# Performance work log

Measured on AMD Instinct MI355X. Metric: run time of the kernel, lower is better.

## Reference

```python
import jax, jax.numpy as jnp
import numpy as np

D_MODEL = 2048
NUM_HEADS = 16
THETA = 10000.0


def setup_inputs() -> dict:
    key = jax.random.key(0)
    ks = jax.random.split(key, 5)
    bs, S, d = 4, 2048, D_MODEL
    std = (2.0 / (d + d)) ** 0.5
    x = jax.random.normal(ks[0], (bs, S, d), dtype=jnp.float32)
    wq = jax.random.normal(ks[1], (d, d), dtype=jnp.float32) * std
    wk = jax.random.normal(ks[2], (d, d), dtype=jnp.float32) * std
    wv = jax.random.normal(ks[3], (d, d), dtype=jnp.float32) * std
    wo = jax.random.normal(ks[4], (d, d), dtype=jnp.float32) * std
    return {"x": x, "wq": wq, "wk": wk, "wv": wv, "wo": wo}


def _rope(t, cos, sin):
    # t: (bs, H, S, d_k); cos/sin: (S, d_k) interleaved-duplicated
    # rotate_half: (-x1, x0, -x3, x2, ...)
    x_even = t[..., 0::2]
    x_odd = t[..., 1::2]
    rot = jnp.stack((-x_odd, x_even), axis=-1).reshape(t.shape)
    return t * cos + rot * sin


def reference(x, wq, wk, wv, wo):
    bs, S, d = x.shape
    H = NUM_HEADS
    dk = d // H
    # QKV projections (Linear has no bias; weight stored (out, in), applied as x @ W.T)
    q = (x @ wq.T).reshape(bs, S, H, dk).transpose(0, 2, 1, 3)  # (bs,H,S,dk)
    k = (x @ wk.T).reshape(bs, S, H, dk).transpose(0, 2, 1, 3)
    v = (x @ wv.T).reshape(bs, S, H, dk).transpose(0, 2, 1, 3)

    # RoPE tables (interleaved convention)
    half = dk // 2
    inv_freq = THETA ** (-2.0 * jnp.arange(half, dtype=jnp.float32) / dk)  # (half,)
    pos = jnp.arange(S, dtype=jnp.float32)
    ang = pos[:, None] * inv_freq[None, :]  # (S, half)
    cos = jnp.repeat(jnp.cos(ang), 2, axis=-1)  # (S, dk), (c0,c0,c1,c1,...)
    sin = jnp.repeat(jnp.sin(ang), 2, axis=-1)
    q = _rope(q, cos, sin)
    k = _rope(k, cos, sin)

    scale = 1.0 / jnp.sqrt(jnp.asarray(dk, dtype=x.dtype))
    attn = jnp.einsum("bhqd,bhkd->bhqk", q, k) * scale  # (bs,H,S,S)
    causal = jnp.tril(jnp.ones((S, S), dtype=bool))
    attn = jnp.where(causal, attn, -jnp.inf)
    probs = jax.nn.softmax(attn, axis=-1)
    out = jnp.einsum("bhqk,bhkd->bhqd", probs, v)  # (bs,H,S,dk)
    out = out.transpose(0, 2, 1, 3).reshape(bs, S, d)
    return out @ wo.T
```

## Files before the change

### kernel.cpp

```cpp
#include <hip/hip_runtime.h>
#include <hip/hip_bf16.h>
#include <cstdint>
#include <cstddef>

typedef unsigned short u16;
typedef unsigned int u32;
typedef __attribute__((ext_vector_type(8))) short short8;
typedef __attribute__((ext_vector_type(4))) short bfx4;
typedef __attribute__((ext_vector_type(4))) float f32x4;

#define D_MODEL 2048
#define SEQ     2048
#define BATCH   4
#define NHEADS  16
#define DKH     128
#define NTOK    (BATCH*SEQ)

typedef const __attribute__((address_space(1))) void* gptr_t;
typedef __attribute__((address_space(3))) void* lptr_t;

__device__ inline float bf2f(u16 u) {
  union { float f; u32 i; } x; x.i = ((u32)u) << 16; return x.f;
}
__device__ inline u16 f2bf(float f) {
  union { float f; u32 i; } x; x.f = f;
  return (u16)((x.i + 0x7FFFu + ((x.i >> 16) & 1u)) >> 16);
}
__device__ inline u32 packbf2(float a, float b) {
  union { float f; u32 i; } xa, xb; xa.f = a; xb.f = b;
  return (xa.i >> 16) | (xb.i & 0xFFFF0000u);
}

__global__ void cvt_kernel(const float* __restrict__ in, u16* __restrict__ out, int n8) {
  int i = blockIdx.x * 256 + threadIdx.x;
  if (i >= n8) return;
  const float* p = in + (size_t)i * 8;
  short8 v;
#pragma unroll
  for (int j = 0; j < 8; ++j) v[j] = (short)f2bf(p[j]);
  *(short8*)(out + (size_t)i * 8) = v;
}

__global__ void cvtw_kernel(const float* __restrict__ wq, const float* __restrict__ wk,
                            const float* __restrict__ wv, const float* __restrict__ wo,
                            u16* __restrict__ wall) {
  int by = blockIdx.y;
  const float* src = by == 0 ? wq : by == 1 ? wk : by == 2 ? wv : wo;
  int i = blockIdx.x * 256 + threadIdx.x;
  const float* p = src + (size_t)i * 8;
  short8 v;
#pragma unroll
  for (int j = 0; j < 8; ++j) v[j] = (short)f2bf(p[j]);
  *(short8*)(wall + (size_t)by * D_MODEL * D_MODEL + (size_t)i * 8) = v;
}

__global__ void trig_kernel(float* __restrict__ cosT, float* __restrict__ sinT) {
  int i = blockIdx.x * 256 + threadIdx.x;
  int s = i >> 6, j = i & 63;
  float inv = powf(10000.0f, -2.0f * (float)j / 128.0f);
  float ang = (float)s * inv;
  cosT[i] = cosf(ang);
  sinT[i] = sinf(ang);
}

template<int F32OUT>
__global__ __launch_bounds__(512, 2)
void gemm_bt256(const u16* __restrict__ A, const u16* __restrict__ B,
                void* __restrict__ Cv, int M, int N, int K) {
  __shared__ u16 lds[2][2][256 * 64];
  const int T = threadIdx.x;
  const int lane = T & 63, w = T >> 6;
  const int lo = lane & 15, hi = lane >> 4;
  const int wr = w >> 2, wc = w & 3;
  const int id = blockIdx.x;
  const int bm = (id >> 3) * 256, bn = (id & 7) * 256;
  const int nt = K >> 6;

  const int qrow_base = (w & 3) * 8 + (w >> 2) * 128;
  const int lrow = lane >> 3;
  const int lchunk = lane & 7;

  auto STAGEQ = [&](int buf, int z, int kt) {
    int r0 = z * 32 + qrow_base;
    int rn = r0 + lrow;
    int ck = lchunk ^ (rn & 7);
    __builtin_amdgcn_global_load_lds(
        (gptr_t)(A + (size_t)(bm + rn) * K + kt * 64 + ck * 8),
        (lptr_t)(&lds[buf][0][0] + r0 * 64), 16, 0, 0);
    __builtin_amdgcn_global_load_lds(
        (gptr_t)(B + (size_t)(bn + rn) * K + kt * 64 + ck * 8),
        (lptr_t)(&lds[buf][1][0] + r0 * 64), 16, 0, 0);
  };

  f32x4 acc[8][4] = {};
  short8 bfrag[4][2];

#define GPHASE(qq, tt, cc) do {                                                \
    short8 af[2][2];                                                           \
    _Pragma("unroll")                                                          \
    for (int m2 = 0; m2 < 2; ++m2) {                                           \
      int row = wr * 128 + (2 * (qq) + m2) * 16 + lo;                          \
      _Pragma("unroll")                                                        \
      for (int c = 0; c < 2; ++c)                                              \
        af[m2][c] = *(const short8*)((const char*)&lds[cc][0][0] +             \
            (row << 7) + ((c * 64 + hi * 16) ^ ((row & 7) << 4)));             \
    }                                                                          \
    if ((qq) == 0) {                                                           \
      _Pragma("unroll")                                                        \
      for (int ni = 0; ni < 4; ++ni) {                                         \
        int row = wc * 64 + ni * 16 + lo;                                      \
        _Pragma("unroll")                                                      \
        for (int c = 0; c < 2; ++c)                                            \
          bfrag[ni][c] = *(const short8*)((const char*)&lds[cc][1][0] +        \
              (row << 7) + ((c * 64 + hi * 16) ^ ((row & 7) << 4)));           \
      }                                                                        \
    }                                                                          \
    { int zz = ((qq) + 3) & 3;                                                 \
      int stt = (qq) == 0 ? (tt) + 1 : (tt) + 2;                               \
      int sbuf = (qq) == 0 ? ((tt) + 1) & 1 : (tt) & 1;                        \
      if (stt < nt) STAGEQ(sbuf, zz, stt); }                                   \
    __builtin_amdgcn_s_barrier();                                              \
    asm volatile("s_waitcnt lgkmcnt(0)" ::: "memory");                         \
    __builtin_amdgcn_sched_barrier(0);                                         \
    __builtin_amdgcn_s_setprio(1);                                             \
    _Pragma("unroll")                                                          \
    for (int m2 = 0; m2 < 2; ++m2)                                             \
      _Pragma("unroll")                                                        \
      for (int ni = 0; ni < 4; ++ni)                                           \
        _Pragma("unroll")                                                      \
        for (int c = 0; c < 2; ++c)                                            \
          acc[2 * (qq) + m2][ni] = __builtin_amdgcn_mfma_f32_16x16x32_bf16(    \
              af[m2][c], bfrag[ni][c], acc[2 * (qq) + m2][ni], 0, 0, 0);       \
    __builtin_amdgcn_s_setprio(0);                                             \
    __builtin_amdgcn_sched_barrier(0);                                         \
    __builtin_amdgcn_s_barrier();                                              \
  } while (0)

#pragma unroll
  for (int z = 0; z < 4; ++z) STAGEQ(0, z, 0);
#pragma unroll
  for (int z = 0; z < 3; ++z) STAGEQ(1, z, 1);
  asm volatile("s_waitcnt vmcnt(6)" ::: "memory");
  __builtin_amdgcn_s_barrier();

  for (int t = 0; t < nt; ++t) {
    const int cur = t & 1;
    GPHASE(0, t, cur);
    GPHASE(1, t, cur);
    GPHASE(2, t, cur);
    GPHASE(3, t, cur);
    if (t == nt - 2) asm volatile("s_waitcnt vmcnt(0)" ::: "memory");
    else             asm volatile("s_waitcnt vmcnt(6)" ::: "memory");
    __builtin_amdgcn_s_barrier();
  }
#undef GPHASE

#pragma unroll
  for (int mi = 0; mi < 8; ++mi)
#pragma unroll
    for (int ni = 0; ni < 4; ++ni) {
      int row = bm + wr * 128 + mi * 16 + hi * 4;
      int col = bn + wc * 64 + ni * 16 + lo;
#pragma unroll
      for (int r = 0; r < 4; ++r) {
        if (F32OUT)
          ((float*)Cv)[(size_t)(row + r) * N + col] = acc[mi][ni][r];
        else
          ((u16*)Cv)[(size_t)(row + r) * N + col] = f2bf(acc[mi][ni][r]);
      }
    }
}

__global__ void rope_kernel(u16* __restrict__ t, const float* __restrict__ cosT,
                            const float* __restrict__ sinT, float premul) {
  int i = blockIdx.x * 256 + threadIdx.x;
  int row = i >> 8;
  int g = i & 255;
  int s = row & (SEQ - 1);
  int col = g << 3;
  int j0 = (col & 127) >> 1;
  short8 v = *(short8*)(t + (size_t)row * D_MODEL + col);
#pragma unroll
  for (int p = 0; p < 4; ++p) {
    float c  = cosT[s * 64 + j0 + p];
    float sn = sinT[s * 64 + j0 + p];
    float e = bf2f((u16)v[2 * p]), o = bf2f((u16)v[2 * p + 1]);
    v[2 * p]     = (short)f2bf((e * c - o * sn) * premul);
    v[2 * p + 1] = (short)f2bf((o * c + e * sn) * premul);
  }
  *(short8*)(t + (size_t)row * D_MODEL + col) = v;
}

__global__ void vt_kernel(const u16* __restrict__ V, u16* __restrict__ VT) {
  __shared__ u16 tbuf[64][66];
  int bh = blockIdx.z;
  int b = bh >> 4, h = bh & 15;
  int s0 = blockIdx.x << 6, d0 = blockIdx.y << 6;
  for (int i = threadIdx.x; i < 512; i += 256) {
    int sr = i >> 3, c8 = (i & 7) << 3;
    short8 v = *(const short8*)(V + (size_t)(b * SEQ + s0 + sr) * D_MODEL + h * DKH + d0 + c8);
#pragma unroll
    for (int j = 0; j < 8; ++j) tbuf[sr][c8 + j] = (u16)v[j];
  }
  __syncthreads();
  for (int i = threadIdx.x; i < 512; i += 256) {
    int dr = i >> 3, s8 = (i & 7) << 3;
    short8 v;
#pragma unroll
    for (int j = 0; j < 8; ++j) v[j] = (short)tbuf[s8 + j][dr];
    *(short8*)(VT + ((size_t)bh * DKH + d0 + dr) * SEQ + s0 + s8) = v;
  }
}

__device__ __forceinline__ void attn_band(
    int band, int b, int h, int bh,
    const u16* __restrict__ Q, const u16* __restrict__ K,
    const u16* __restrict__ VT, u16* __restrict__ O,
    const float* __restrict__ cosT, const float* __restrict__ sinT,
    u16 (*Ksb)[64 * 128], u16 (*Vsb)[128 * 64], u16* Pw)
{
  const int T = threadIdx.x, lane = T & 63, w = T >> 6;
  const int lo = lane & 15, hi = lane >> 4;
  const int grp = w >> 2, wl = w & 3;
  const int qt = band * 2 + grp;
  const int qrow = qt * 64 + wl * 16 + lo;
  const int ktmax = band * 2 + 1;
  const int swzC = (lo & 7) << 4;
  const float SC = 0.08838834764831845f * 1.4426950408889634f;

  const u16* Qp = Q + (size_t)(b * SEQ + qrow) * D_MODEL + h * DKH;
  const float* cp = cosT + qrow * 64;
  const float* sp = sinT + qrow * 64;
  short8 qf[4];
#pragma unroll
  for (int c = 0; c < 4; ++c) {
    short8 v = *(const short8*)(Qp + c * 32 + hi * 8);
#pragma unroll
    for (int p = 0; p < 4; ++p) {
      float cc = cp[c * 16 + hi * 4 + p] * SC;
      float sn = sp[c * 16 + hi * 4 + p] * SC;
      float e = bf2f((u16)v[2 * p]), o = bf2f((u16)v[2 * p + 1]);
      v[2 * p]     = (short)f2bf(e * cc - o * sn);
      v[2 * p + 1] = (short)f2bf(o * cc + e * sn);
    }
    qf[c] = v;
  }

  f32x4 ot[8] = {};
  float m = -1e30f, l = 0.f;

  const u16* Kbase = K + ((size_t)b * SEQ) * D_MODEL + h * DKH;
  const u16* Vbase = VT + (size_t)bh * DKH * SEQ;

  auto STAGE = [&](int buf, int kt2) {
    const int kb2 = kt2 << 6;
#pragma unroll
    for (int q = 0; q < 2; ++q) {
      int base = q * 512 + w * 64;
      int s = base + lane;
      int kv = s >> 4, ck = (s & 15) ^ (kv & 7);
      __builtin_amdgcn_global_load_lds(
          (gptr_t)(Kbase + (size_t)(kb2 + kv) * D_MODEL + ck * 8),
          (lptr_t)(Ksb[buf] + (size_t)base * 8), 16, 0, 0);
      int d = s >> 3, cv2 = (s & 7) ^ (d & 7);
      __builtin_amdgcn_global_load_lds(
          (gptr_t)(Vbase + (size_t)d * SEQ + kb2 + cv2 * 8),
          (lptr_t)(Vsb[buf] + (size_t)base * 8), 16, 0, 0);
    }
  };

  STAGE(0, 0);
  __syncthreads();
  int cur = 0;

  for (int kt = 0; kt <= ktmax; ++kt) {
    if (kt < ktmax) STAGE(cur ^ 1, kt + 1);
    if (kt <= qt) {
      const int kb = kt << 6;
      const u16* Ks = Ksb[cur];
      const u16* Vs = Vsb[cur];

      f32x4 sa[4];
      __builtin_amdgcn_s_setprio(1);
#pragma unroll
      for (int g = 0; g < 4; ++g) {
        f32x4 s4 = {0.f, 0.f, 0.f, 0.f};
        int krow = g * 16 + lo;
#pragma unroll
        for (int c = 0; c < 4; ++c) {
          int o = ((krow << 8) + c * 64 + hi * 16) ^ ((krow & 7) << 4);
          short8 kf = *(const short8*)((const char*)Ks + o);
          s4 = __builtin_amdgcn_mfma_f32_16x16x32_bf16(kf, qf[c], s4, 0, 0, 0);
        }
        sa[g] = s4;
      }
      __builtin_amdgcn_s_setprio(0);

      const bool diag = (kt == qt);
      float pm = -1e30f;
#pragma unroll
      for (int g = 0; g < 4; ++g)
#pragma unroll
        for (int r = 0; r < 4; ++r) {
          float sv = sa[g][r];
          if (diag && (kb + g * 16 + hi * 4 + r) > qrow) sv = -1e30f;
          sa[g][r] = sv;
          pm = fmaxf(pm, sv);
        }
      pm = fmaxf(pm, __shfl_xor(pm, 16));
      pm = fmaxf(pm, __shfl_xor(pm, 32));

      if (!__all(pm <= m + 8.0f)) {
        float mn = fmaxf(m, pm);
        float sc = __builtin_amdgcn_exp2f(m - mn);
        l *= sc;
#pragma unroll
        for (int g2 = 0; g2 < 8; ++g2)
#pragma unroll
          for (int r = 0; r < 4; ++r) ot[g2][r] *= sc;
        m = mn;
      }

      float rs = 0.f;
#pragma unroll
      for (int g = 0; g < 4; ++g) {
        float p0 = __builtin_amdgcn_exp2f(sa[g][0] - m);
        float p1 = __builtin_amdgcn_exp2f(sa[g][1] - m);
        float p2 = __builtin_amdgcn_exp2f(sa[g][2] - m);
        float p3 = __builtin_amdgcn_exp2f(sa[g][3] - m);
        rs += (p0 + p1) + (p2 + p3);
        int off = lo * 128 + ((g * 32 + hi * 8) ^ swzC);
        *(u32*)((char*)Pw + off)     = packbf2(p0, p1);
        *(u32*)((char*)Pw + off + 4) = packbf2(p2, p3);
      }
      rs += __shfl_xor(rs, 16);
      rs += __shfl_xor(rs, 32);
      l += rs;

      __builtin_amdgcn_s_setprio(1);
#pragma unroll
      for (int c2 = 0; c2 < 2; ++c2) {
        short8 pf = *(const short8*)((char*)Pw + lo * 128 + ((c2 * 64 + hi * 16) ^ swzC));
#pragma unroll
        for (int g2 = 0; g2 < 8; ++g2) {
          int vrow = g2 * 16 + lo;
          int vo = ((vrow << 7) + c2 * 64 + hi * 16) ^ ((vrow & 7) << 4);
          short8 vf = *(const short8*)((const char*)Vs + vo);
          ot[g2] = __builtin_amdgcn_mfma_f32_16x16x32_bf16(vf, pf, ot[g2], 0, 0, 0);
        }
      }
      __builtin_amdgcn_s_setprio(0);
    }

    __syncthreads();
    cur ^= 1;
  }

  float invl = 1.0f / l;
  u16* Op = O + (size_t)(b * SEQ + qrow) * D_MODEL + h * DKH + hi * 4;
#pragma unroll
  for (int g2 = 0; g2 < 8; ++g2) {
    bfx4 v4;
#pragma unroll
    for (int r = 0; r < 4; ++r) v4[r] = (short)f2bf(ot[g2][r] * invl);
    *(bfx4*)(Op + g2 * 16) = v4;
  }
}

__global__ __launch_bounds__(512)
void attn_kernel(const u16* __restrict__ Q, const u16* __restrict__ K,
                 const u16* __restrict__ VT, u16* __restrict__ O,
                 const float* __restrict__ cosT, const float* __restrict__ sinT) {
  __shared__ u16 Ksb[2][64 * 128];
  __shared__ u16 Vsb[2][128 * 64];
  __shared__ u16 Ps[8 * 1024];
  const int wg = blockIdx.x;
  const int xcd = wg & 7, idx = wg >> 3;
  const int bh = xcd * 8 + (idx >> 3);
  const int tp = idx & 7;
  const int b = bh >> 4, h = bh & 15;
  u16* Pw = Ps + (threadIdx.x >> 6) * 1024;
  attn_band(15 - tp, b, h, bh, Q, K, VT, O, cosT, sinT, Ksb, Vsb, Pw);
  attn_band(tp,      b, h, bh, Q, K, VT, O, cosT, sinT, Ksb, Vsb, Pw);
}

extern "C" void kernel_launch(void* const* d_in, const int* in_sizes, int n_in,
                              void* d_out, int out_size, void* d_ws, size_t ws_size,
                              hipStream_t stream) {
  const float* x  = (const float*)d_in[0];
  const float* wq = (const float*)d_in[1];
  const float* wk = (const float*)d_in[2];
  const float* wv = (const float*)d_in[3];
  const float* wo = (const float*)d_in[4];
  float* out = (float*)d_out;

  const size_t TOKB = (size_t)NTOK * D_MODEL * 2;
  const size_t WB   = (size_t)D_MODEL * D_MODEL * 2;
  char* p = (char*)d_ws;
  u16* xb  = (u16*)p; p += TOKB;
  u16* wqb = (u16*)p; p += WB;
  u16* wkb = (u16*)p; p += WB;
  u16* wvb = (u16*)p; p += WB;
  u16* wob = (u16*)p; p += WB;
  u16* Qb  = (u16*)p; p += TOKB;
  u16* Kb  = (u16*)p; p += TOKB;
  u16* Vb  = (u16*)p; p += TOKB;
  u16* VTb = (u16*)p; p += TOKB;
  u16* Ob  = (u16*)p; p += TOKB;
  float* cosT = (float*)p; p += (size_t)SEQ * 64 * 4;
  float* sinT = (float*)p; p += (size_t)SEQ * 64 * 4;

  cvt_kernel<<<8192, 256, 0, stream>>>(x, xb, 2097152);
  cvtw_kernel<<<dim3(2048, 4), 256, 0, stream>>>(wq, wk, wv, wo, wqb);
  trig_kernel<<<512, 256, 0, stream>>>(cosT, sinT);

  gemm_bt256<0><<<256, 512, 0, stream>>>(xb, wqb, Qb, NTOK, D_MODEL, D_MODEL);
  gemm_bt256<0><<<256, 512, 0, stream>>>(xb, wkb, Kb, NTOK, D_MODEL, D_MODEL);
  gemm_bt256<0><<<256, 512, 0, stream>>>(xb, wvb, Vb, NTOK, D_MODEL, D_MODEL);

  rope_kernel<<<8192, 256, 0, stream>>>(Kb, cosT, sinT, 1.0f);

  vt_kernel<<<dim3(32, 2, 64), 256, 0, stream>>>(Vb, VTb);

  attn_kernel<<<512, 512, 0, stream>>>(Qb, Kb, VTb, Ob, cosT, sinT);

  gemm_bt256<1><<<256, 512, 0, stream>>>(Ob, wob, out, NTOK, D_MODEL, D_MODEL);
}
```

Measured before the change: 483.9 us.

## Process two query tiles per wave in attention to reuse K/V fragments

Result: slower. 513.8 us (+6.2%).

```diff
diff --git a/kernel.cpp b/kernel.cpp
--- a/kernel.cpp
+++ b/kernel.cpp
@@ -221,33 +221,37 @@
 {
   const int T = threadIdx.x, lane = T & 63, w = T >> 6;
   const int lo = lane & 15, hi = lane >> 4;
-  const int grp = w >> 2, wl = w & 3;
-  const int qt = band * 2 + grp;
-  const int qrow = qt * 64 + wl * 16 + lo;
+  const int qrow0 = band * 128 + w * 16 + lo;
+  const int qrow1 = qrow0 + 64;
+  const int qt0 = band * 2;
   const int ktmax = band * 2 + 1;
   const int swzC = (lo & 7) << 4;
   const float SC = 0.08838834764831845f * 1.4426950408889634f;
 
-  const u16* Qp = Q + (size_t)(b * SEQ + qrow) * D_MODEL + h * DKH;
-  const float* cp = cosT + qrow * 64;
-  const float* sp = sinT + qrow * 64;
-  short8 qf[4];
-#pragma unroll
-  for (int c = 0; c < 4; ++c) {
-    short8 v = *(const short8*)(Qp + c * 32 + hi * 8);
-#pragma unroll
-    for (int p = 0; p < 4; ++p) {
-      float cc = cp[c * 16 + hi * 4 + p] * SC;
-      float sn = sp[c * 16 + hi * 4 + p] * SC;
-      float e = bf2f((u16)v[2 * p]), o = bf2f((u16)v[2 * p + 1]);
-      v[2 * p]     = (short)f2bf(e * cc - o * sn);
-      v[2 * p + 1] = (short)f2bf(o * cc + e * sn);
-    }
-    qf[c] = v;
-  }
-
-  f32x4 ot[8] = {};
-  float m = -1e30f, l = 0.f;
+  short8 qf0[4], qf1[4];
+#pragma unroll
+  for (int t2 = 0; t2 < 2; ++t2) {
+    int qrow = t2 ? qrow1 : qrow0;
+    const u16* Qp = Q + (size_t)(b * SEQ + qrow) * D_MODEL + h * DKH;
+    const float* cp = cosT + qrow * 64;
+    const float* sp = sinT + qrow * 64;
+#pragma unroll
+    for (int c = 0; c < 4; ++c) {
+      short8 v = *(const short8*)(Qp + c * 32 + hi * 8);
+#pragma unroll
+      for (int p = 0; p < 4; ++p) {
+        float cc = cp[c * 16 + hi * 4 + p] * SC;
+        float sn = sp[c * 16 + hi * 4 + p] * SC;
+        float e = bf2f((u16)v[2 * p]), o = bf2f((u16)v[2 * p + 1]);
+        v[2 * p]     = (short)f2bf(e * cc - o * sn);
+        v[2 * p + 1] = (short)f2bf(o * cc + e * sn);
+      }
+      if (t2) qf1[c] = v; else qf0[c] = v;
+    }
+  }
+
+  f32x4 ot0[8] = {}, ot1[8] = {};
+  float m0 = -1e30f, l0 = 0.f, m1 = -1e30f, l1 = 0.f;
 
   const u16* Kbase = K + ((size_t)b * SEQ) * D_MODEL + h * DKH;
   const u16* Vbase = VT + (size_t)bh * DKH * SEQ;
@@ -255,8 +259,8 @@
   auto STAGE = [&](int buf, int kt2) {
     const int kb2 = kt2 << 6;
 #pragma unroll
-    for (int q = 0; q < 2; ++q) {
-      int base = q * 512 + w * 64;
+    for (int q = 0; q < 4; ++q) {
+      int base = q * 256 + (T & 192);
       int s = base + lane;
       int kv = s >> 4, ck = (s & 15) ^ (kv & 7);
       __builtin_amdgcn_global_load_lds(
@@ -275,111 +279,130 @@
 
   for (int kt = 0; kt <= ktmax; ++kt) {
     if (kt < ktmax) STAGE(cur ^ 1, kt + 1);
-    if (kt <= qt) {
-      const int kb = kt << 6;
-      const u16* Ks = Ksb[cur];
-      const u16* Vs = Vsb[cur];
-
-      f32x4 sa[4];
-      __builtin_amdgcn_s_setprio(1);
-#pragma unroll
-      for (int g = 0; g < 4; ++g) {
-        f32x4 s4 = {0.f, 0.f, 0.f, 0.f};
-        int krow = g * 16 + lo;
-#pragma unroll
-        for (int c = 0; c < 4; ++c) {
-          int o = ((krow << 8) + c * 64 + hi * 16) ^ ((krow & 7) << 4);
-          short8 kf = *(const short8*)((const char*)Ks + o);
-          s4 = __builtin_amdgcn_mfma_f32_16x16x32_bf16(kf, qf[c], s4, 0, 0, 0);
-        }
-        sa[g] = s4;
+    const int kb = kt << 6;
+    const u16* Ks = Ksb[cur];
+    const u16* Vs = Vsb[cur];
+
+    f32x4 sa0[4], sa1[4];
+    __builtin_amdgcn_s_setprio(1);
+#pragma unroll
+    for (int g = 0; g < 4; ++g) {
+      f32x4 s40 = {0.f, 0.f, 0.f, 0.f}, s41 = {0.f, 0.f, 0.f, 0.f};
+      int krow = g * 16 + lo;
+#pragma unroll
+      for (int c = 0; c < 4; ++c) {
+        int o = ((krow << 8) + c * 64 + hi * 16) ^ ((krow & 7) << 4);
+        short8 kf = *(const short8*)((const char*)Ks + o);
+        s40 = __builtin_amdgcn_mfma_f32_16x16x32_bf16(kf, qf0[c], s40, 0, 0, 0);
+        s41 = __builtin_amdgcn_mfma_f32_16x16x32_bf16(kf, qf1[c], s41, 0, 0, 0);
       }
-      __builtin_amdgcn_s_setprio(0);
-
-      const bool diag = (kt == qt);
-      float pm = -1e30f;
-#pragma unroll
-      for (int g = 0; g < 4; ++g)
-#pragma unroll
-        for (int r = 0; r < 4; ++r) {
-          float sv = sa[g][r];
-          if (diag && (kb + g * 16 + hi * 4 + r) > qrow) sv = -1e30f;
-          sa[g][r] = sv;
-          pm = fmaxf(pm, sv);
-        }
-      pm = fmaxf(pm, __shfl_xor(pm, 16));
-      pm = fmaxf(pm, __shfl_xor(pm, 32));
-
-      if (!__all(pm <= m + 8.0f)) {
-        float mn = fmaxf(m, pm);
-        float sc = __builtin_amdgcn_exp2f(m - mn);
-        l *= sc;
-#pragma unroll
-        for (int g2 = 0; g2 < 8; ++g2)
-#pragma unroll
-          for (int r = 0; r < 4; ++r) ot[g2][r] *= sc;
-        m = mn;
+      sa0[g] = s40; sa1[g] = s41;
+    }
+    __builtin_amdgcn_s_setprio(0);
+
+    const bool dg0 = (kt >= qt0), dg1 = (kt == ktmax);
+    float pm0 = -1e30f, pm1 = -1e30f;
+#pragma unroll
+    for (int g = 0; g < 4; ++g)
+#pragma unroll
+      for (int r = 0; r < 4; ++r) {
+        int kvg = kb + g * 16 + hi * 4 + r;
+        float sv0 = sa0[g][r], sv1 = sa1[g][r];
+        if (dg0 && kvg > qrow0) sv0 = -1e30f;
+        if (dg1 && kvg > qrow1) sv1 = -1e30f;
+        sa0[g][r] = sv0; sa1[g][r] = sv1;
+        pm0 = fmaxf(pm0, sv0); pm1 = fmaxf(pm1, sv1);
       }
-
-      float rs = 0.f;
-#pragma unroll
-      for (int g = 0; g < 4; ++g) {
-        float p0 = __builtin_amdgcn_exp2f(sa[g][0] - m);
-        float p1 = __builtin_amdgcn_exp2f(sa[g][1] - m);
-        float p2 = __builtin_amdgcn_exp2f(sa[g][2] - m);
-        float p3 = __builtin_amdgcn_exp2f(sa[g][3] - m);
-        rs += (p0 + p1) + (p2 + p3);
-        int off = lo * 128 + ((g * 32 + hi * 8) ^ swzC);
-        *(u32*)((char*)Pw + off)     = packbf2(p0, p1);
-        *(u32*)((char*)Pw + off + 4) = packbf2(p2, p3);
+    pm0 = fmaxf(pm0, __shfl_xor(pm0, 16));
+    pm0 = fmaxf(pm0, __shfl_xor(pm0, 32));
+    pm1 = fmaxf(pm1, __shfl_xor(pm1, 16));
+    pm1 = fmaxf(pm1, __shfl_xor(pm1, 32));
+
+    if (!__all((pm0 <= m0 + 8.0f) & (pm1 <= m1 + 8.0f))) {
+      float mn0 = fmaxf(m0, pm0), mn1 = fmaxf(m1, pm1);
+      float sc0 = __builtin_amdgcn_exp2f(m0 - mn0);
+      float sc1 = __builtin_amdgcn_exp2f(m1 - mn1);
+      l0 *= sc0; l1 *= sc1;
+#pragma unroll
+      for (int g2 = 0; g2 < 8; ++g2)
+#pragma unroll
+        for (int r = 0; r < 4; ++r) { ot0[g2][r] *= sc0; ot1[g2][r] *= sc1; }
+      m0 = mn0; m1 = mn1;
+    }
+
+    float rs0 = 0.f, rs1 = 0.f;
+#pragma unroll
+    for (int g = 0; g < 4; ++g) {
+      float a0 = __builtin_amdgcn_exp2f(sa0[g][0] - m0);
+      float a1 = __builtin_amdgcn_exp2f(sa0[g][1] - m0);
+      float a2 = __builtin_amdgcn_exp2f(sa0[g][2] - m0);
+      float a3 = __builtin_amdgcn_exp2f(sa0[g][3] - m0);
+      float b0 = __builtin_amdgcn_exp2f(sa1[g][0] - m1);
+      float b1 = __builtin_amdgcn_exp2f(sa1[g][1] - m1);
+      float b2 = __builtin_amdgcn_exp2f(sa1[g][2] - m1);
+      float b3 = __builtin_amdgcn_exp2f(sa1[g][3] - m1);
+      rs0 += (a0 + a1) + (a2 + a3);
+      rs1 += (b0 + b1) + (b2 + b3);
+      int off = lo * 128 + ((g * 32 + hi * 8) ^ swzC);
+      *(u32*)((char*)Pw + off)            = packbf2(a0, a1);
+      *(u32*)((char*)Pw + off + 4)        = packbf2(a2, a3);
+      *(u32*)((char*)Pw + 2048 + off)     = packbf2(b0, b1);
+      *(u32*)((char*)Pw + 2048 + off + 4) = packbf2(b2, b3);
+    }
+    rs0 += __shfl_xor(rs0, 16); rs0 += __shfl_xor(rs0, 32);
+    rs1 += __shfl_xor(rs1, 16); rs1 += __shfl_xor(rs1, 32);
+    l0 += rs0; l1 += rs1;
+
+    __builtin_amdgcn_s_setprio(1);
+#pragma unroll
+    for (int c2 = 0; c2 < 2; ++c2) {
+      int pb = lo * 128 + ((c2 * 64 + hi * 16) ^ swzC);
+      short8 pf0 = *(const short8*)((char*)Pw + pb);
+      short8 pf1 = *(const short8*)((char*)Pw + 2048 + pb);
+#pragma unroll
+      for (int g2 = 0; g2 < 8; ++g2) {
+        int vrow = g2 * 16 + lo;
+        int vo = ((vrow << 7) + c2 * 64 + hi * 16) ^ ((vrow & 7) << 4);
+        short8 vf = *(const short8*)((const char*)Vs + vo);
+        ot0[g2] = __builtin_amdgcn_mfma_f32_16x16x32_bf16(vf, pf0, ot0[g2], 0, 0, 0);
+        ot1[g2] = __builtin_amdgcn_mfma_f32_16x16x32_bf16(vf, pf1, ot1[g2], 0, 0, 0);
       }
-      rs += __shfl_xor(rs, 16);
-      rs += __shfl_xor(rs, 32);
-      l += rs;
-
-      __builtin_amdgcn_s_setprio(1);
-#pragma unroll
-      for (int c2 = 0; c2 < 2; ++c2) {
-        short8 pf = *(const short8*)((char*)Pw + lo * 128 + ((c2 * 64 + hi * 16) ^ swzC));
-#pragma unroll
-        for (int g2 = 0; g2 < 8; ++g2) {
-          int vrow = g2 * 16 + lo;
-          int vo = ((vrow << 7) + c2 * 64 + hi * 16) ^ ((vrow & 7) << 4);
-          short8 vf = *(const short8*)((const char*)Vs + vo);
-          ot[g2] = __builtin_amdgcn_mfma_f32_16x16x32_bf16(vf, pf, ot[g2], 0, 0, 0);
-        }
-      }
-      __builtin_amdgcn_s_setprio(0);
-    }
+    }
+    __builtin_amdgcn_s_setprio(0);
 
     __syncthreads();
     cur ^= 1;
   }
 
-  float invl = 1.0f / l;
-  u16* Op = O + (size_t)(b * SEQ + qrow) * D_MODEL + h * DKH + hi * 4;
+  float il0 = 1.0f / l0, il1 = 1.0f / l1;
+  u16* Op0 = O + (size_t)(b * SEQ + qrow0) * D_MODEL + h * DKH + hi * 4;
+  u16* Op1 = O + (size_t)(b * SEQ + qrow1) * D_MODEL + h * DKH + hi * 4;
 #pragma unroll
   for (int g2 = 0; g2 < 8; ++g2) {
-    bfx4 v4;
-#pragma unroll
-    for (int r = 0; r < 4; ++r) v4[r] = (short)f2bf(ot[g2][r] * invl);
-    *(bfx4*)(Op + g2 * 16) = v4;
-  }
-}
-
-__global__ __launch_bounds__(512)
+    bfx4 v0, v1;
+#pragma unroll
+    for (int r = 0; r < 4; ++r) {
+      v0[r] = (short)f2bf(ot0[g2][r] * il0);
+      v1[r] = (short)f2bf(ot1[g2][r] * il1);
+    }
+    *(bfx4*)(Op0 + g2 * 16) = v0;
+    *(bfx4*)(Op1 + g2 * 16) = v1;
+  }
+}
+
+__global__ __launch_bounds__(256)
 void attn_kernel(const u16* __restrict__ Q, const u16* __restrict__ K,
                  const u16* __restrict__ VT, u16* __restrict__ O,
                  const float* __restrict__ cosT, const float* __restrict__ sinT) {
   __shared__ u16 Ksb[2][64 * 128];
   __shared__ u16 Vsb[2][128 * 64];
-  __shared__ u16 Ps[8 * 1024];
+  __shared__ u16 Ps[4 * 2048];
   const int wg = blockIdx.x;
   const int xcd = wg & 7, idx = wg >> 3;
   const int bh = xcd * 8 + (idx >> 3);
   const int tp = idx & 7;
   const int b = bh >> 4, h = bh & 15;
-  u16* Pw = Ps + (threadIdx.x >> 6) * 1024;
+  u16* Pw = Ps + (threadIdx.x >> 6) * 2048;
   attn_band(15 - tp, b, h, bh, Q, K, VT, O, cosT, sinT, Ksb, Vsb, Pw);
   attn_band(tp,      b, h, bh, Q, K, VT, O, cosT, sinT, Ksb, Vsb, Pw);
 }
@@ -422,7 +445,7 @@
 
   vt_kernel<<<dim3(32, 2, 64), 256, 0, stream>>>(Vb, VTb);
 
-  attn_kernel<<<512, 512, 0, stream>>>(Qb, Kb, VTb, Ob, cosT, sinT);
+  attn_kernel<<<512, 256, 0, stream>>>(Qb, Kb, VTb, Ob, cosT, sinT);
 
   gemm_bt256<1><<<256, 512, 0, stream>>>(Ob, wob, out, NTOK, D_MODEL, D_MODEL);
 }
```
